# Kernel optimization log

Measured on AMD Instinct MI355X. Metric: run time of the kernel, lower is better.

Reference implementation:

```python
import jax, jax.numpy as jnp
import numpy as np

D, DK, DV, H = 1024, 64, 1024, 16
DVH = DV // H  # per-head value dim
EPS = 1e-5


def _layer_norm(x, g, b):
    mu = jnp.mean(x, axis=-1, keepdims=True)
    var = jnp.var(x, axis=-1, keepdims=True)
    return (x - mu) * jax.lax.rsqrt(var + EPS) * g + b


def setup_inputs() -> dict:
    key = jax.random.key(0)
    ks = jax.random.split(key, 12)
    s = lambda k, shape, fan_in: jax.random.normal(k, shape, jnp.float32) / np.sqrt(fan_in)
    return {
        "x": jax.random.normal(ks[0], (2, 2048, D), jnp.float32),
        "Wq": s(ks[1], (H, D, DK), D),
        "Wk": s(ks[2], (H, D, DK), D),
        "Wv": s(ks[3], (H, D, DVH), D),
        "Wo": s(ks[4], (DV, D), DV),
        "ln1_g": jnp.ones((D,), jnp.float32),
        "ln1_b": jnp.zeros((D,), jnp.float32),
        "W1": s(ks[5], (D, 4 * D), D),
        "b1": jnp.zeros((4 * D,), jnp.float32),
        "W2": s(ks[6], (4 * D, D), 4 * D),
        "b2": jnp.zeros((D,), jnp.float32),
        "ln2_g": jnp.ones((D,), jnp.float32),
        "ln2_b": jnp.zeros((D,), jnp.float32),
    }


def reference(x, Wq, Wk, Wv, Wo, ln1_g, ln1_b, W1, b1, W2, b2, ln2_g, ln2_b):
    B, S, _ = x.shape
    # per-head projections (vectorized over the head loop of the original)
    q = jnp.einsum("bsd,hdk->bhsk", x, Wq)
    k = jnp.einsum("bsd,hdk->bhsk", x, Wk)
    v = jnp.einsum("bsd,hdv->bhsv", x, Wv)
    scores = jnp.einsum("bhsk,bhtk->bhst", q, k) / np.sqrt(DK).astype(np.float32)
    attn = jax.nn.softmax(scores, axis=-1)
    o = jnp.einsum("bhst,bhtv->bhsv", attn, v)  # [B,H,S,DVH]
    o = o.transpose(0, 2, 1, 3).reshape(B, S, DV)  # concat heads
    attn_out = o @ Wo
    x1 = _layer_norm(attn_out + x, ln1_g, ln1_b)
    ffn = jax.nn.relu(x1 @ W1 + b1) @ W2 + b2
    return _layer_norm(ffn + x1, ln2_g, ln2_b)
```

## Files before the change

### kernel.cpp

```cpp
#include <hip/hip_runtime.h>
#include <hip/hip_bf16.h>

typedef unsigned short u16;
typedef unsigned int u32;
typedef short short8 __attribute__((ext_vector_type(8)));
typedef float fx4 __attribute__((ext_vector_type(4)));
typedef u32 ux4 __attribute__((ext_vector_type(4)));
typedef u32 ux2 __attribute__((ext_vector_type(2)));

__device__ __forceinline__ float b2f(u16 x) {
  return __uint_as_float(((u32)x) << 16);
}
__device__ __forceinline__ u16 f2b(float f) {
  u32 u = __float_as_uint(f);
  u += 0x7fffu + ((u >> 16) & 1u);
  return (u16)(u >> 16);
}
__device__ __forceinline__ u32 cvtpk(float a, float b) {
  u32 r;
  asm("v_cvt_pk_bf16_f32 %0, %1, %2" : "=v"(r) : "v"(a), "v"(b));
  return r;
}
__device__ __forceinline__ short8 scale8(short8 v, float s) {
  u32 r0 = cvtpk(b2f((u16)v[0]) * s, b2f((u16)v[1]) * s);
  u32 r1 = cvtpk(b2f((u16)v[2]) * s, b2f((u16)v[3]) * s);
  u32 r2 = cvtpk(b2f((u16)v[4]) * s, b2f((u16)v[5]) * s);
  u32 r3 = cvtpk(b2f((u16)v[6]) * s, b2f((u16)v[7]) * s);
  return __builtin_bit_cast(short8, ux4{r0, r1, r2, r3});
}

__device__ __forceinline__ void load16(const u16* g, u16* l) {
  __builtin_amdgcn_global_load_lds(
      (__attribute__((address_space(1))) void*)(u16*)g,
      (__attribute__((address_space(3))) void*)l, 16, 0, 0);
}

__global__ __launch_bounds__(256) void cvt_f2b_kernel(
    const float* __restrict__ in, u16* __restrict__ out)
{
  int i = (blockIdx.x * 256 + threadIdx.x) * 4;
  fx4 v = *(const fx4*)(in + i);
  u16 o4[4];
#pragma unroll
  for (int j = 0; j < 4; ++j) o4[j] = f2b(v[j]);
  *(uint2*)(out + i) = *(uint2*)o4;
}

__global__ __launch_bounds__(256) void transpose_f2b_kernel(
    const float* __restrict__ in, u16* __restrict__ out,
    int R, int C, int out_ld)
{
  __shared__ __align__(16) u16 tile[32][33];
  int tx = threadIdx.x, ty = threadIdx.y;
  int c0 = blockIdx.x * 32, r0 = blockIdx.y * 32;
  const float* inb = in + (size_t)blockIdx.z * R * C;
  u16* outb = out + (size_t)blockIdx.z * C * out_ld;
#pragma unroll
  for (int i = 0; i < 4; ++i)
    tile[ty + i * 8][tx] = f2b(inb[(size_t)(r0 + ty + i * 8) * C + c0 + tx]);
  __syncthreads();
#pragma unroll
  for (int i = 0; i < 4; ++i)
    outb[(size_t)(c0 + ty + i * 8) * out_ld + r0 + tx] = tile[tx][ty + i * 8];
}

__global__ __launch_bounds__(256) void transpose_b2b_kernel(
    const u16* __restrict__ in, u16* __restrict__ out, int in_ld, int out_ld)
{
  __shared__ __align__(16) u16 tile[32][33];
  int tx = threadIdx.x, ty = threadIdx.y;
  int c0 = blockIdx.x * 32, r0 = blockIdx.y * 32;
#pragma unroll
  for (int i = 0; i < 4; ++i)
    tile[ty + i * 8][tx] = in[(size_t)(r0 + ty + i * 8) * in_ld + c0 + tx];
  __syncthreads();
#pragma unroll
  for (int i = 0; i < 4; ++i)
    out[(size_t)(c0 + ty + i * 8) * out_ld + r0 + tx] = tile[tx][ty + i * 8];
}

__global__ __launch_bounds__(256, 2) void gemm_bt(
    const u16* __restrict__ A, const u16* __restrict__ BT,
    const float* __restrict__ bias, void* __restrict__ Cp,
    int M, int N, int K, int flags)
{
  __shared__ __align__(16) u16 As[2][4096];
  __shared__ __align__(16) u16 Bs[2][4096];
  int tid = threadIdx.x;
  int lane = tid & 63, wid = tid >> 6;
  int l15 = lane & 15, quad = lane >> 4;
  int wm = wid >> 1, wn = wid & 1;
  int m0 = blockIdx.y * 128, n0 = blockIdx.x * 128;

  int srow = wid * 16 + (lane >> 2);
  int sswz = (((lane >> 2) & 3) + ((lane >> 4) & 3)) & 3;
  int gch = (lane & 3) ^ sswz;
  const u16* gA = A + (size_t)(m0 + srow) * K + gch * 8;
  const u16* gB = BT + (size_t)(n0 + srow) * K + gch * 8;
  size_t gstep = (size_t)64 * K;
  u16* lA = &As[0][wid * 512];
  u16* lB = &Bs[0][wid * 512];

  int rswz = ((l15 & 3) + (l15 >> 2)) & 3;
  int rphys = ((quad ^ rswz) & 3) << 3;

  fx4 acc[4][4];
#pragma unroll
  for (int i = 0; i < 4; ++i)
#pragma unroll
    for (int j = 0; j < 4; ++j) acc[i][j] = fx4{0.f, 0.f, 0.f, 0.f};

  int nt = K >> 5;
  load16(gA,         lA);
  load16(gA + gstep, lA + 2048);
  load16(gB,         lB);
  load16(gB + gstep, lB + 2048);

  for (int kt = 0; kt < nt; ++kt) {
    __syncthreads();
    if (kt + 1 < nt) {
      int buf = (kt + 1) & 1;
      const u16* ga = gA + (kt + 1) * 32;
      const u16* gb = gB + (kt + 1) * 32;
      load16(ga,         lA + buf * 4096);
      load16(ga + gstep, lA + buf * 4096 + 2048);
      load16(gb,         lB + buf * 4096);
      load16(gb + gstep, lB + buf * 4096 + 2048);
    }
    const u16* Ab = As[kt & 1];
    const u16* Bb = Bs[kt & 1];
    short8 af[4], bf[4];
#pragma unroll
    for (int t = 0; t < 4; ++t)
      af[t] = *(const short8*)&Ab[(wm * 64 + t * 16 + l15) * 32 + rphys];
#pragma unroll
    for (int t = 0; t < 4; ++t)
      bf[t] = *(const short8*)&Bb[(wn * 64 + t * 16 + l15) * 32 + rphys];
#pragma unroll
    for (int tm = 0; tm < 4; ++tm)
#pragma unroll
      for (int tn = 0; tn < 4; ++tn)
        acc[tm][tn] = __builtin_amdgcn_mfma_f32_16x16x32_bf16(
            af[tm], bf[tn], acc[tm][tn], 0, 0, 0);
  }

  bool obf = flags & 1, hb = flags & 2, rl = flags & 4;
#pragma unroll
  for (int tn = 0; tn < 4; ++tn) {
    int col = n0 + wn * 64 + tn * 16 + l15;
    float bv = hb ? bias[col] : 0.0f;
#pragma unroll
    for (int tm = 0; tm < 4; ++tm) {
      int row = m0 + wm * 64 + tm * 16 + (quad << 2);
#pragma unroll
      for (int r = 0; r < 4; ++r) {
        float v = acc[tm][tn][r] + bv;
        if (rl) v = fmaxf(v, 0.0f);
        size_t idx = (size_t)(row + r) * N + col;
        if (obf) ((u16*)Cp)[idx] = f2b(v);
        else ((float*)Cp)[idx] = v;
      }
    }
  }
}

__global__ __launch_bounds__(256, 2) void gemm_bt_k64(
    const u16* __restrict__ A, const u16* __restrict__ BT,
    const float* __restrict__ bias, void* __restrict__ Cp,
    int M, int N, int K, int flags)
{
  __shared__ __align__(16) u16 As[2][8192];
  __shared__ __align__(16) u16 Bs[2][8192];
  int tid = threadIdx.x;
  int lane = tid & 63, wid = tid >> 6;
  int l15 = lane & 15, quad = lane >> 4;
  int wm = wid >> 1, wn = wid & 1;

  int bx = blockIdx.x, by = blockIdx.y, bz = blockIdx.z;
  if (gridDim.z > 1) {
    int nx = gridDim.x, ny = gridDim.y;
    int total = nx * ny * (int)gridDim.z;
    int cpx = total >> 3;
    int lin = bx + nx * (by + ny * bz);
    int swb = (lin & 7) * cpx + (lin >> 3);
    bx = swb % nx;
    int t2 = swb / nx;
    by = t2 % ny;
    bz = t2 / ny;
  }
  int m0 = by * 128, n0 = bx * 128;
  int kc = K / (int)gridDim.z;

  int r8 = lane >> 3;
  int clog = (lane & 7) ^ r8;
  const u16* gA = A + (size_t)(m0 + wid * 8 + r8) * K + bz * kc + clog * 8;
  const u16* gB = BT + (size_t)(n0 + wid * 8 + r8) * K + bz * kc + clog * 8;
  size_t gstep = (size_t)32 * K;
  u16* lA = &As[0][wid * 512];
  u16* lB = &Bs[0][wid * 512];

  fx4 acc[4][4];
#pragma unroll
  for (int i = 0; i < 4; ++i)
#pragma unroll
    for (int j = 0; j < 4; ++j) acc[i][j] = fx4{0.f, 0.f, 0.f, 0.f};

  int nt = kc >> 6;
#pragma unroll
  for (int i = 0; i < 4; ++i) {
    load16(gA + i * gstep, lA + i * 2048);
    load16(gB + i * gstep, lB + i * 2048);
  }

  for (int kt = 0; kt < nt; ++kt) {
    __syncthreads();
    if (kt + 1 < nt) {
      int buf = (kt + 1) & 1;
      const u16* ga = gA + (kt + 1) * 64;
      const u16* gb = gB + (kt + 1) * 64;
#pragma unroll
      for (int i = 0; i < 4; ++i) {
        load16(ga + i * gstep, lA + buf * 8192 + i * 2048);
        load16(gb + i * gstep, lB + buf * 8192 + i * 2048);
      }
    }
    const u16* Ab = As[kt & 1];
    const u16* Bb = Bs[kt & 1];
#pragma unroll
    for (int s = 0; s < 2; ++s) {
      int ch = (((s << 2) | quad) ^ (l15 & 7)) << 3;
      short8 af[4], bf[4];
#pragma unroll
      for (int t = 0; t < 4; ++t)
        af[t] = *(const short8*)&Ab[(wm * 64 + t * 16 + l15) * 64 + ch];
#pragma unroll
      for (int t = 0; t < 4; ++t)
        bf[t] = *(const short8*)&Bb[(wn * 64 + t * 16 + l15) * 64 + ch];
#pragma unroll
      for (int tm = 0; tm < 4; ++tm)
#pragma unroll
        for (int tn = 0; tn < 4; ++tn)
          acc[tm][tn] = __builtin_amdgcn_mfma_f32_16x16x32_bf16(
              af[tm], bf[tn], acc[tm][tn], 0, 0, 0);
    }
  }

  bool obf = flags & 1, hb = flags & 2, rl = flags & 4;
  u16* cb16 = (u16*)Cp + (size_t)bz * M * N;
  float* cf32 = (float*)Cp + (size_t)bz * M * N;
#pragma unroll
  for (int tn = 0; tn < 4; ++tn) {
    int col = n0 + wn * 64 + tn * 16 + l15;
    float bv = hb ? bias[col] : 0.0f;
#pragma unroll
    for (int tm = 0; tm < 4; ++tm) {
      int row = m0 + wm * 64 + tm * 16 + (quad << 2);
#pragma unroll
      for (int r = 0; r < 4; ++r) {
        float v = acc[tm][tn][r] + bv;
        if (rl) v = fmaxf(v, 0.0f);
        size_t idx = (size_t)(row + r) * N + col;
        if (obf) cb16[idx] = f2b(v);
        else cf32[idx] = v;
      }
    }
  }
}

__global__ __launch_bounds__(256, 2) void attn_kernel(
    const u16* __restrict__ qkv, const u16* __restrict__ vT,
    u16* __restrict__ o)
{
  __shared__ __align__(16) u16 Ks[2][8192];
  __shared__ __align__(16) u16 Vs[2][8192];
  int tid = threadIdx.x;
  int lane = tid & 63, wid = tid >> 6;
  int l15 = lane & 15, quad = lane >> 4;
  int b = blockIdx.z, h = blockIdx.y;
  int q0 = blockIdx.x * 128 + wid * 32;

  const float SC = 0.18033688011112042f;
  const u16* qbA = qkv + (size_t)(b * 2048 + q0 + l15) * 3072 + h * 64 + (quad << 3);
  short8 qA0 = scale8(*(const short8*)qbA, SC);
  short8 qA1 = scale8(*(const short8*)(qbA + 32), SC);
  const u16* qbB = qbA + (size_t)16 * 3072;
  short8 qB0 = scale8(*(const short8*)qbB, SC);
  short8 qB1 = scale8(*(const short8*)(qbB + 32), SC);

  int srow = tid >> 3;
  int gc8 = ((tid & 7) ^ (srow & 7)) << 3;
  const u16* kg = qkv + (size_t)(b * 2048 + srow) * 3072 + 1024 + h * 64 + gc8;
  const u16* vg = vT + (size_t)(h * 64 + srow) * 4096 + b * 2048 + gc8;
  u16* lk = &Ks[0][wid * 512];
  u16* lv = &Vs[0][wid * 512];

  int lq = l15 >> 2;
  int rs = ((((lq & 1) << 1) | (lq >> 1)) << 2) | (l15 & 3);
  int sk = rs & 7;

  fx4 oaccA[4], oaccB[4];
  float sumA = 0.0f, sumB = 0.0f;
#pragma unroll
  for (int i = 0; i < 4; ++i) {
    oaccA[i] = fx4{0.f, 0.f, 0.f, 0.f};
    oaccB[i] = fx4{0.f, 0.f, 0.f, 0.f};
  }

#pragma unroll
  for (int j = 0; j < 4; ++j)
    load16(kg + (size_t)j * 32 * 3072, lk + j * 2048);
#pragma unroll
  for (int st = 0; st < 2; ++st)
#pragma unroll
    for (int dh = 0; dh < 2; ++dh)
      load16(vg + st * 64 + (size_t)dh * 32 * 4096, lv + st * 4096 + dh * 2048);

  int swz = l15 & 7;
  for (int kt = 0; kt < 16; ++kt) {
    __syncthreads();
    if (kt + 1 < 16) {
      int buf = (kt + 1) & 1;
      const u16* kgn = kg + (size_t)(kt + 1) * 128 * 3072;
      const u16* vgn = vg + (kt + 1) * 128;
#pragma unroll
      for (int j = 0; j < 4; ++j)
        load16(kgn + (size_t)j * 32 * 3072, lk + buf * 8192 + j * 2048);
#pragma unroll
      for (int st = 0; st < 2; ++st)
#pragma unroll
        for (int dh = 0; dh < 2; ++dh)
          load16(vgn + st * 64 + (size_t)dh * 32 * 4096,
                 lv + buf * 8192 + st * 4096 + dh * 2048);
    }
    const u16* Kb = Ks[kt & 1];
    const u16* Vb = Vs[kt & 1];

#pragma unroll
    for (int st = 0; st < 2; ++st) {
      const u16* Kbs = Kb + st * 4096;
      const u16* Vbs = Vb + st * 4096;

      fx4 scA[4], scB[4];
      __builtin_amdgcn_s_setprio(1);
#pragma unroll
      for (int sub = 0; sub < 4; ++sub) {
        const u16* rp = &Kbs[(sub * 16 + rs) * 64];
        short8 kf0 = *(const short8*)&rp[((quad ^ sk) & 7) << 3];
        short8 kf1 = *(const short8*)&rp[(((4 | quad) ^ sk) & 7) << 3];
        scA[sub] = fx4{0.f, 0.f, 0.f, 0.f};
        scA[sub] = __builtin_amdgcn_mfma_f32_16x16x32_bf16(kf0, qA0, scA[sub], 0, 0, 0);
        scA[sub] = __builtin_amdgcn_mfma_f32_16x16x32_bf16(kf1, qA1, scA[sub], 0, 0, 0);
        scB[sub] = fx4{0.f, 0.f, 0.f, 0.f};
        scB[sub] = __builtin_amdgcn_mfma_f32_16x16x32_bf16(kf0, qB0, scB[sub], 0, 0, 0);
        scB[sub] = __builtin_amdgcn_mfma_f32_16x16x32_bf16(kf1, qB1, scB[sub], 0, 0, 0);
      }
      __builtin_amdgcn_s_setprio(0);

      u32 WA[4][2], WB[4][2];
      float psA = 0.0f, psB = 0.0f;
#pragma unroll
      for (int sub = 0; sub < 4; ++sub) {
        float a0 = __builtin_amdgcn_exp2f(scA[sub][0]);
        float a1 = __builtin_amdgcn_exp2f(scA[sub][1]);
        float a2 = __builtin_amdgcn_exp2f(scA[sub][2]);
        float a3 = __builtin_amdgcn_exp2f(scA[sub][3]);
        psA += (a0 + a1) + (a2 + a3);
        WA[sub][0] = cvtpk(a0, a1);
        WA[sub][1] = cvtpk(a2, a3);
        float b0 = __builtin_amdgcn_exp2f(scB[sub][0]);
        float b1 = __builtin_amdgcn_exp2f(scB[sub][1]);
        float b2 = __builtin_amdgcn_exp2f(scB[sub][2]);
        float b3 = __builtin_amdgcn_exp2f(scB[sub][3]);
        psB += (b0 + b1) + (b2 + b3);
        WB[sub][0] = cvtpk(b0, b1);
        WB[sub][1] = cvtpk(b2, b3);
      }
      sumA += psA;
      sumB += psB;

      ux2 eA00 = __builtin_amdgcn_permlane32_swap(WA[0][0], WA[1][0], false, false);
      ux2 eA01 = __builtin_amdgcn_permlane32_swap(WA[0][1], WA[1][1], false, false);
      ux2 eA10 = __builtin_amdgcn_permlane32_swap(WA[2][0], WA[3][0], false, false);
      ux2 eA11 = __builtin_amdgcn_permlane32_swap(WA[2][1], WA[3][1], false, false);
      short8 pa1A = __builtin_bit_cast(short8, ux4{eA00[0], eA01[0], eA00[1], eA01[1]});
      short8 pa2A = __builtin_bit_cast(short8, ux4{eA10[0], eA11[0], eA10[1], eA11[1]});
      ux2 eB00 = __builtin_amdgcn_permlane32_swap(WB[0][0], WB[1][0], false, false);
      ux2 eB01 = __builtin_amdgcn_permlane32_swap(WB[0][1], WB[1][1], false, false);
      ux2 eB10 = __builtin_amdgcn_permlane32_swap(WB[2][0], WB[3][0], false, false);
      ux2 eB11 = __builtin_amdgcn_permlane32_swap(WB[2][1], WB[3][1], false, false);
      short8 pa1B = __builtin_bit_cast(short8, ux4{eB00[0], eB01[0], eB00[1], eB01[1]});
      short8 pa2B = __builtin_bit_cast(short8, ux4{eB10[0], eB11[0], eB10[1], eB11[1]});

      __builtin_amdgcn_s_setprio(1);
#pragma unroll
      for (int dt = 0; dt < 4; ++dt) {
        const u16* rp = &Vbs[(dt * 16 + l15) * 64];
        short8 vf0 = *(const short8*)&rp[((quad ^ swz) & 7) << 3];
        short8 vf1 = *(const short8*)&rp[(((4 | quad) ^ swz) & 7) << 3];
        oaccA[dt] = __builtin_amdgcn_mfma_f32_16x16x32_bf16(pa1A, vf0, oaccA[dt], 0, 0, 0);
        oaccA[dt] = __builtin_amdgcn_mfma_f32_16x16x32_bf16(pa2A, vf1, oaccA[dt], 0, 0, 0);
        oaccB[dt] = __builtin_amdgcn_mfma_f32_16x16x32_bf16(pa1B, vf0, oaccB[dt], 0, 0, 0);
        oaccB[dt] = __builtin_amdgcn_mfma_f32_16x16x32_bf16(pa2B, vf1, oaccB[dt], 0, 0, 0);
      }
      __builtin_amdgcn_s_setprio(0);
    }
  }
  sumA += __shfl_xor(sumA, 16, 64);
  sumA += __shfl_xor(sumA, 32, 64);
  sumB += __shfl_xor(sumB, 16, 64);
  sumB += __shfl_xor(sumB, 32, 64);
  fx4 invA, invB;
#pragma unroll
  for (int r = 0; r < 4; ++r) {
    invA[r] = 1.0f / __shfl(sumA, (quad << 2) + r, 64);
    invB[r] = 1.0f / __shfl(sumB, (quad << 2) + r, 64);
  }
#pragma unroll
  for (int dt = 0; dt < 4; ++dt) {
    int col = h * 64 + dt * 16 + l15;
#pragma unroll
    for (int r = 0; r < 4; ++r) {
      size_t rowA = (size_t)(b * 2048 + q0 + (quad << 2) + r);
      o[rowA * 1024 + col] = f2b(oaccA[dt][r] * invA[r]);
      o[(rowA + 16) * 1024 + col] = f2b(oaccB[dt][r] * invB[r]);
    }
  }
}

__global__ __launch_bounds__(256) void ln_kernel(
    const float* __restrict__ main0, const float* __restrict__ main1,
    const float* __restrict__ res, const float* __restrict__ cbias,
    const float* __restrict__ g, const float* __restrict__ beta,
    u16* __restrict__ out_b, float* __restrict__ out_f)
{
  __shared__ float red[8];
  int row = blockIdx.x, tid = threadIdx.x;
  size_t base = (size_t)row * 1024 + tid * 4;
  fx4 v = *(const fx4*)(main0 + base);
  fx4 v1 = *(const fx4*)(main1 + base);
  fx4 rv = *(const fx4*)(res + base);
#pragma unroll
  for (int i = 0; i < 4; ++i) v[i] += v1[i] + rv[i];
  if (cbias) {
    fx4 cb = *(const fx4*)(cbias + tid * 4);
#pragma unroll
    for (int i = 0; i < 4; ++i) v[i] += cb[i];
  }
  float s = v[0] + v[1] + v[2] + v[3];
  float sq = v[0] * v[0] + v[1] * v[1] + v[2] * v[2] + v[3] * v[3];
#pragma unroll
  for (int off = 32; off >= 1; off >>= 1) {
    s += __shfl_xor(s, off, 64);
    sq += __shfl_xor(sq, off, 64);
  }
  int wid = tid >> 6, lane = tid & 63;
  if (lane == 0) { red[wid] = s; red[wid + 4] = sq; }
  __syncthreads();
  float S = red[0] + red[1] + red[2] + red[3];
  float SQ = red[4] + red[5] + red[6] + red[7];
  float mean = S * (1.0f / 1024.0f);
  float var = SQ * (1.0f / 1024.0f) - mean * mean;
  float rs = rsqrtf(var + 1e-5f);
  fx4 gv = *(const fx4*)(g + tid * 4);
  fx4 bv = *(const fx4*)(beta + tid * 4);
  float of[4];
#pragma unroll
  for (int i = 0; i < 4; ++i) of[i] = (v[i] - mean) * rs * gv[i] + bv[i];
  if (out_f) *(fx4*)(out_f + base) = *(const fx4*)of;
  if (out_b) {
    u16 o4[4];
#pragma unroll
    for (int i = 0; i < 4; ++i) o4[i] = f2b(of[i]);
    *(uint2*)(out_b + base) = *(uint2*)o4;
  }
}

extern "C" void kernel_launch(void* const* d_in, const int* in_sizes, int n_in,
                              void* d_out, int out_size, void* d_ws, size_t ws_size,
                              hipStream_t stream) {
  (void)in_sizes; (void)n_in; (void)out_size; (void)ws_size;
  const float* x     = (const float*)d_in[0];
  const float* Wq    = (const float*)d_in[1];
  const float* Wk    = (const float*)d_in[2];
  const float* Wv    = (const float*)d_in[3];
  const float* Wo    = (const float*)d_in[4];
  const float* g1    = (const float*)d_in[5];
  const float* bb1   = (const float*)d_in[6];
  const float* W1    = (const float*)d_in[7];
  const float* bias1 = (const float*)d_in[8];
  const float* W2    = (const float*)d_in[9];
  const float* bias2 = (const float*)d_in[10];
  const float* g2    = (const float*)d_in[11];
  const float* bb2   = (const float*)d_in[12];

  char* ws = (char*)d_ws;
  const size_t MB = 1048576;
  u16* xb     = (u16*)(ws);
  u16* wqkvT  = (u16*)(ws + 8 * MB);
  u16* woT    = (u16*)(ws + 38 * MB);
  u16* qkv    = (u16*)(ws + 40 * MB);
  u16* vT     = (u16*)(ws + 64 * MB);
  u16* ob     = (u16*)(ws + 72 * MB);
  float* aout = (float*)(ws);
  u16* x1     = (u16*)(ws + 64 * MB);
  float* x1f  = (float*)(ws + 40 * MB);
  u16* w1T    = (u16*)(ws + 56 * MB);
  u16* w2T    = (u16*)(ws);
  u16* hbuf   = (u16*)(ws + 8 * MB);
  float* ffn  = (float*)(ws + 56 * MB);

  dim3 tb(32, 8, 1);
  cvt_f2b_kernel<<<4096, 256, 0, stream>>>(x, xb);
  transpose_f2b_kernel<<<dim3(2, 32, 16), tb, 0, stream>>>(Wq, wqkvT,           1024, 64, 1024);
  transpose_f2b_kernel<<<dim3(2, 32, 16), tb, 0, stream>>>(Wk, wqkvT + 1048576, 1024, 64, 1024);
  transpose_f2b_kernel<<<dim3(2, 32, 16), tb, 0, stream>>>(Wv, wqkvT + 2097152, 1024, 64, 1024);
  transpose_f2b_kernel<<<dim3(32, 32, 1), tb, 0, stream>>>(Wo, woT, 1024, 1024, 1024);

  gemm_bt<<<dim3(24, 32), 256, 0, stream>>>(xb, wqkvT, nullptr, qkv, 4096, 3072, 1024, 1);
  transpose_b2b_kernel<<<dim3(32, 128), tb, 0, stream>>>(qkv + 2048, vT, 3072, 4096);
  attn_kernel<<<dim3(16, 16, 2), 256, 0, stream>>>(qkv, vT, ob);
  gemm_bt_k64<<<dim3(8, 32, 2), 256, 0, stream>>>(ob, woT, nullptr, aout, 4096, 1024, 1024, 0);
  ln_kernel<<<4096, 256, 0, stream>>>(aout, aout + 4194304, x, nullptr, g1, bb1, x1, x1f);
  transpose_f2b_kernel<<<dim3(128, 32, 1), tb, 0, stream>>>(W1, w1T, 1024, 4096, 1024);
  transpose_f2b_kernel<<<dim3(32, 128, 1), tb, 0, stream>>>(W2, w2T, 4096, 1024, 4096);
  gemm_bt_k64<<<dim3(32, 32, 1), 256, 0, stream>>>(x1, w1T, bias1, hbuf, 4096, 4096, 1024, 1 | 2 | 4);
  gemm_bt_k64<<<dim3(8, 32, 2), 256, 0, stream>>>(hbuf, w2T, nullptr, ffn, 4096, 1024, 4096, 0);
  ln_kernel<<<4096, 256, 0, stream>>>(ffn, ffn + 4194304, x1f, bias2, g2, bb2, nullptr, (float*)d_out);
}
```

Before: 348.7 us.

## Switch GEMM to triple-buffered K=32 pipeline with explicit vmcnt waits

```diff
diff --git a/kernel.cpp b/kernel.cpp
--- a/kernel.cpp
+++ b/kernel.cpp
@@ -164,13 +164,13 @@
   }
 }
 
-__global__ __launch_bounds__(256, 2) void gemm_bt_k64(
+__global__ __launch_bounds__(256, 2) void gemm_bt_p3(
     const u16* __restrict__ A, const u16* __restrict__ BT,
     const float* __restrict__ bias, void* __restrict__ Cp,
     int M, int N, int K, int flags)
 {
-  __shared__ __align__(16) u16 As[2][8192];
-  __shared__ __align__(16) u16 Bs[2][8192];
+  __shared__ __align__(16) u16 As[3][4096];
+  __shared__ __align__(16) u16 Bs[3][4096];
   int tid = threadIdx.x;
   int lane = tid & 63, wid = tid >> 6;
   int l15 = lane & 15, quad = lane >> 4;
@@ -191,13 +191,15 @@
   int m0 = by * 128, n0 = bx * 128;
   int kc = K / (int)gridDim.z;
 
-  int r8 = lane >> 3;
-  int clog = (lane & 7) ^ r8;
-  const u16* gA = A + (size_t)(m0 + wid * 8 + r8) * K + bz * kc + clog * 8;
-  const u16* gB = BT + (size_t)(n0 + wid * 8 + r8) * K + bz * kc + clog * 8;
-  size_t gstep = (size_t)32 * K;
-  u16* lA = &As[0][wid * 512];
-  u16* lB = &Bs[0][wid * 512];
+  int srow = wid * 16 + (lane >> 2);
+  int sswz = (((lane >> 2) & 3) + ((lane >> 4) & 3)) & 3;
+  int gch = (lane & 3) ^ sswz;
+  const u16* gA = A + (size_t)(m0 + srow) * K + bz * kc + gch * 8;
+  const u16* gB = BT + (size_t)(n0 + srow) * K + bz * kc + gch * 8;
+  size_t gstep = (size_t)64 * K;
+
+  int rswz = ((l15 & 3) + (l15 >> 2)) & 3;
+  int rphys = ((quad ^ rswz) & 3) << 3;
 
   fx4 acc[4][4];
 #pragma unroll
@@ -205,44 +207,45 @@
 #pragma unroll
     for (int j = 0; j < 4; ++j) acc[i][j] = fx4{0.f, 0.f, 0.f, 0.f};
 
-  int nt = kc >> 6;
-#pragma unroll
-  for (int i = 0; i < 4; ++i) {
-    load16(gA + i * gstep, lA + i * 2048);
-    load16(gB + i * gstep, lB + i * 2048);
-  }
-
+  int nt = kc >> 5;
+  auto issue = [&](int t, int buf) {
+    const u16* ga = gA + t * 32;
+    const u16* gb = gB + t * 32;
+    u16* la = &As[buf][wid * 512];
+    u16* lb = &Bs[buf][wid * 512];
+    load16(ga,         la);
+    load16(ga + gstep, la + 2048);
+    load16(gb,         lb);
+    load16(gb + gstep, lb + 2048);
+  };
+  issue(0, 0);
+  if (nt > 1) issue(1, 1);
+
+  int cur = 0, pre = 2;
   for (int kt = 0; kt < nt; ++kt) {
-    __syncthreads();
-    if (kt + 1 < nt) {
-      int buf = (kt + 1) & 1;
-      const u16* ga = gA + (kt + 1) * 64;
-      const u16* gb = gB + (kt + 1) * 64;
-#pragma unroll
-      for (int i = 0; i < 4; ++i) {
-        load16(ga + i * gstep, lA + buf * 8192 + i * 2048);
-        load16(gb + i * gstep, lB + buf * 8192 + i * 2048);
-      }
-    }
-    const u16* Ab = As[kt & 1];
-    const u16* Bb = Bs[kt & 1];
-#pragma unroll
-    for (int s = 0; s < 2; ++s) {
-      int ch = (((s << 2) | quad) ^ (l15 & 7)) << 3;
-      short8 af[4], bf[4];
-#pragma unroll
-      for (int t = 0; t < 4; ++t)
-        af[t] = *(const short8*)&Ab[(wm * 64 + t * 16 + l15) * 64 + ch];
-#pragma unroll
-      for (int t = 0; t < 4; ++t)
-        bf[t] = *(const short8*)&Bb[(wn * 64 + t * 16 + l15) * 64 + ch];
-#pragma unroll
-      for (int tm = 0; tm < 4; ++tm)
-#pragma unroll
-        for (int tn = 0; tn < 4; ++tn)
-          acc[tm][tn] = __builtin_amdgcn_mfma_f32_16x16x32_bf16(
-              af[tm], bf[tn], acc[tm][tn], 0, 0, 0);
-    }
+    __builtin_amdgcn_sched_barrier(0);
+    if (kt + 1 < nt) asm volatile("s_waitcnt vmcnt(4)" ::: "memory");
+    else             asm volatile("s_waitcnt vmcnt(0)" ::: "memory");
+    __builtin_amdgcn_s_barrier();
+    __builtin_amdgcn_sched_barrier(0);
+    if (kt + 2 < nt) issue(kt + 2, pre);
+    const u16* Ab = As[cur];
+    const u16* Bb = Bs[cur];
+    short8 af[4], bf[4];
+#pragma unroll
+    for (int t = 0; t < 4; ++t)
+      af[t] = *(const short8*)&Ab[(wm * 64 + t * 16 + l15) * 32 + rphys];
+#pragma unroll
+    for (int t = 0; t < 4; ++t)
+      bf[t] = *(const short8*)&Bb[(wn * 64 + t * 16 + l15) * 32 + rphys];
+#pragma unroll
+    for (int tm = 0; tm < 4; ++tm)
+#pragma unroll
+      for (int tn = 0; tn < 4; ++tn)
+        acc[tm][tn] = __builtin_amdgcn_mfma_f32_16x16x32_bf16(
+            af[tm], bf[tn], acc[tm][tn], 0, 0, 0);
+    cur = (cur == 2) ? 0 : cur + 1;
+    pre = (pre == 2) ? 0 : pre + 1;
   }
 
   bool obf = flags & 1, hb = flags & 2, rl = flags & 4;
@@ -519,11 +522,11 @@
   gemm_bt<<<dim3(24, 32), 256, 0, stream>>>(xb, wqkvT, nullptr, qkv, 4096, 3072, 1024, 1);
   transpose_b2b_kernel<<<dim3(32, 128), tb, 0, stream>>>(qkv + 2048, vT, 3072, 4096);
   attn_kernel<<<dim3(16, 16, 2), 256, 0, stream>>>(qkv, vT, ob);
-  gemm_bt_k64<<<dim3(8, 32, 2), 256, 0, stream>>>(ob, woT, nullptr, aout, 4096, 1024, 1024, 0);
+  gemm_bt_p3<<<dim3(8, 32, 2), 256, 0, stream>>>(ob, woT, nullptr, aout, 4096, 1024, 1024, 0);
   ln_kernel<<<4096, 256, 0, stream>>>(aout, aout + 4194304, x, nullptr, g1, bb1, x1, x1f);
   transpose_f2b_kernel<<<dim3(128, 32, 1), tb, 0, stream>>>(W1, w1T, 1024, 4096, 1024);
   transpose_f2b_kernel<<<dim3(32, 128, 1), tb, 0, stream>>>(W2, w2T, 4096, 1024, 4096);
-  gemm_bt_k64<<<dim3(32, 32, 1), 256, 0, stream>>>(x1, w1T, bias1, hbuf, 4096, 4096, 1024, 1 | 2 | 4);
-  gemm_bt_k64<<<dim3(8, 32, 2), 256, 0, stream>>>(hbuf, w2T, nullptr, ffn, 4096, 1024, 4096, 0);
+  gemm_bt_p3<<<dim3(32, 32, 1), 256, 0, stream>>>(x1, w1T, bias1, hbuf, 4096, 4096, 1024, 1 | 2 | 4);
+  gemm_bt_p3<<<dim3(8, 32, 2), 256, 0, stream>>>(hbuf, w2T, nullptr, ffn, 4096, 1024, 4096, 0);
   ln_kernel<<<4096, 256, 0, stream>>>(ffn, ffn + 4194304, x1f, bias2, g2, bb2, nullptr, (float*)d_out);
 }
```

Result: slower. 376.1 us (+7.9%).
